# Performance work log

Hardware: AMD Instinct MI355X
Metric: run time of the kernel (lower is better)

## Reference

```python
import jax, jax.numpy as jnp
import numpy as np
import math

# Config: 8 packed images, each a 32x32 patch grid (t=1) -> equal seglen 1024
NSEG, GH, GW = 8, 32, 32
L = GH * GW            # 1024 tokens per segment
S = NSEG * L           # 8192 packed tokens
H, NH = 1024, 16
HD = H // NH           # 64, head dim (rope dim), divisible by 4
MLP = 4096
THETA = 10000.0


def _make_rope_cos_sin():
    # Rope2DPosEmb._precompute_freqs_cis for a (GH, GW) grid, dim=HD
    flat = np.arange(L, dtype=np.float32)
    x_pos = flat % GW
    y_pos = flat // GW
    dim_range = np.arange(0, HD, 4, dtype=np.float32)[: HD // 4]
    freqs = 1.0 / THETA ** (dim_range / HD)          # [HD//4]
    x_f = np.outer(x_pos, freqs)                     # [L, HD//4]
    y_f = np.outer(y_pos, freqs)
    # interleave x/y angles per frequency -> [L, HD//2]
    ang = np.stack([x_f, y_f], axis=-1).reshape(L, HD // 2)
    ang = np.tile(ang, (NSEG, 1))                    # same grid repeated per image
    return jnp.asarray(np.cos(ang)), jnp.asarray(np.sin(ang))


def setup_inputs() -> dict:
    key = jax.random.key(0)
    ks = jax.random.split(key, 8)
    cos, sin = _make_rope_cos_sin()
    inp = {
        "x": jax.random.normal(ks[0], (S, H), jnp.float32),
        "wqkv": jax.random.normal(ks[1], (3 * H, H), jnp.float32) * math.sqrt(1.0 / H),
        "wo": jax.random.normal(ks[2], (H, H), jnp.float32) * math.sqrt(1.0 / H),
        "ln0_g": jnp.ones((H,), jnp.float32),
        "ln0_b": jnp.zeros((H,), jnp.float32),
        "ln1_g": jnp.ones((H,), jnp.float32),
        "ln1_b": jnp.zeros((H,), jnp.float32),
        "fc0_w": jax.random.normal(ks[3], (MLP, H), jnp.float32) * math.sqrt(2.0 / H),
        "fc0_b": jnp.zeros((MLP,), jnp.float32),
        "fc1_w": jax.random.normal(ks[4], (H, MLP), jnp.float32) * math.sqrt(2.0 / MLP),
        "fc1_b": jnp.zeros((H,), jnp.float32),
        "rope_cos": cos,
        "rope_sin": sin,
        "cu_seqlens": jnp.arange(NSEG + 1, dtype=jnp.int32) * L,
    }
    return inp


def _layernorm(x, g, b, eps=1e-5):
    m = x.mean(-1, keepdims=True)
    v = ((x - m) ** 2).mean(-1, keepdims=True)
    return (x - m) * jax.lax.rsqrt(v + eps) * g + b


def _apply_rope(x, cos, sin):
    # x: [S, NH, HD]; cos/sin: [S, HD//2]. Complex mult on (even, odd) pairs.
    xr = x.reshape(S, NH, HD // 2, 2)
    x0, x1 = xr[..., 0], xr[..., 1]
    c = cos[:, None, :]
    s = sin[:, None, :]
    o0 = x0 * c - x1 * s
    o1 = x0 * s + x1 * c
    return jnp.stack([o0, o1], axis=-1).reshape(S, NH, HD)


def reference(x, wqkv, wo, ln0_g, ln0_b, ln1_g, ln1_b,
              fc0_w, fc0_b, fc1_w, fc1_b, rope_cos, rope_sin, cu_seqlens):
    # --- attention branch (pre-norm) ---
    h = _layernorm(x, ln0_g, ln0_b)
    qkv = (h @ wqkv.T).reshape(S, 3, NH, HD)
    q, k, v = qkv[:, 0], qkv[:, 1], qkv[:, 2]
    q = _apply_rope(q, rope_cos, rope_sin)
    k = _apply_rope(k, rope_cos, rope_sin)
    # block-diagonal varlen attention: equal-length segments -> reshape
    qb = q.reshape(NSEG, L, NH, HD)
    kb = k.reshape(NSEG, L, NH, HD)
    vb = v.reshape(NSEG, L, NH, HD)
    scores = jnp.einsum("blhd,bmhd->bhlm", qb, kb) / math.sqrt(HD)
    p = jax.nn.softmax(scores.astype(jnp.float32), axis=-1).astype(x.dtype)
    attn = jnp.einsum("bhlm,bmhd->blhd", p, vb).reshape(S, H)
    x = x + attn @ wo.T
    # --- MLP branch (pre-norm) ---
    h2 = _layernorm(x, ln1_g, ln1_b)
    mlp = jax.nn.gelu(h2 @ fc0_w.T + fc0_b, approximate=False) @ fc1_w.T + fc1_b
    return x + mlp
```

## Files before the change

kernel.cpp:

```cpp
#include <hip/hip_runtime.h>
#include <math.h>


typedef __bf16 bf16x8 __attribute__((ext_vector_type(8)));
typedef float f32x4 __attribute__((ext_vector_type(4)));
typedef float f32x16 __attribute__((ext_vector_type(16)));
typedef unsigned int u32;

__device__ __forceinline__ unsigned short f2b(float f) {
  unsigned u = __float_as_uint(f);
  return (unsigned short)((u + 0x7FFFu + ((u >> 16) & 1u)) >> 16);
}
__device__ __forceinline__ float b2f(unsigned short h) {
  return __uint_as_float(((unsigned)h) << 16);
}
__device__ __forceinline__ void async_ld16(const void* g, void* l) {
  __builtin_amdgcn_global_load_lds((__attribute__((address_space(1))) void*)g,
                                   (__attribute__((address_space(3))) void*)l,
                                   16, 0, 0);
}
__device__ __forceinline__ float exp2fast(float x) {
#if __has_builtin(__builtin_amdgcn_exp2f)
  return __builtin_amdgcn_exp2f(x);
#else
  return exp2f(x);
#endif
}
__device__ __forceinline__ float rcpfast(float x) {
#if __has_builtin(__builtin_amdgcn_rcpf)
  return __builtin_amdgcn_rcpf(x);
#else
  return 1.0f / x;
#endif
}

__global__ __launch_bounds__(256) void castln_kernel(
    const float* __restrict__ w0, const float* __restrict__ w1,
    const float* __restrict__ w2, const float* __restrict__ w3,
    unsigned short* __restrict__ wdst,
    const float* __restrict__ x, const float* __restrict__ g,
    const float* __restrict__ bt, unsigned short* __restrict__ hout) {
  __shared__ float red[8];
  const int blk = blockIdx.x;
  if (blk < 12288) {
    const int t = blk * 256 + threadIdx.x;
    const float* src;
    int off;
    if (t < 786432) { src = w0; off = t; }
    else if (t < 1048576) { src = w1; off = t - 786432; }
    else if (t < 2097152) { src = w2; off = t - 1048576; }
    else { src = w3; off = t - 2097152; }
    const float4 v = ((const float4*)src)[off];
    ushort4 o;
    o.x = f2b(v.x); o.y = f2b(v.y); o.z = f2b(v.z); o.w = f2b(v.w);
    ((ushort4*)wdst)[t] = o;
    return;
  }
  const int row = blk - 12288, t = threadIdx.x;
  const float4 v = ((const float4*)(x + (size_t)row * 1024))[t];
  float s = v.x + v.y + v.z + v.w;
  float s2 = v.x * v.x + v.y * v.y + v.z * v.z + v.w * v.w;
#pragma unroll
  for (int m = 1; m < 64; m <<= 1) {
    s += __shfl_xor(s, m, 64);
    s2 += __shfl_xor(s2, m, 64);
  }
  if ((t & 63) == 0) { red[t >> 6] = s; red[4 + (t >> 6)] = s2; }
  __syncthreads();
  const float ts = red[0] + red[1] + red[2] + red[3];
  const float ts2 = red[4] + red[5] + red[6] + red[7];
  const float mean = ts * (1.f / 1024.f);
  const float var = ts2 * (1.f / 1024.f) - mean * mean;
  const float inv = rsqrtf(var + 1e-5f);
  const float4 gv = ((const float4*)g)[t];
  const float4 bv = ((const float4*)bt)[t];
  ushort4 o;
  o.x = f2b((v.x - mean) * inv * gv.x + bv.x);
  o.y = f2b((v.y - mean) * inv * gv.y + bv.y);
  o.z = f2b((v.z - mean) * inv * gv.z + bv.z);
  o.w = f2b((v.w - mean) * inv * gv.w + bv.w);
  ((ushort4*)hout)[(size_t)row * 256 + t] = o;
}

__global__ __launch_bounds__(256) void ln_kernel(const float* __restrict__ x,
                                                 const float* __restrict__ g,
                                                 const float* __restrict__ bt,
                                                 unsigned short* __restrict__ out) {
  __shared__ float red[8];
  const int row = blockIdx.x, t = threadIdx.x;
  const float4 v = ((const float4*)(x + (size_t)row * 1024))[t];
  float s = v.x + v.y + v.z + v.w;
  float s2 = v.x * v.x + v.y * v.y + v.z * v.z + v.w * v.w;
#pragma unroll
  for (int m = 1; m < 64; m <<= 1) {
    s += __shfl_xor(s, m, 64);
    s2 += __shfl_xor(s2, m, 64);
  }
  if ((t & 63) == 0) { red[t >> 6] = s; red[4 + (t >> 6)] = s2; }
  __syncthreads();
  const float ts = red[0] + red[1] + red[2] + red[3];
  const float ts2 = red[4] + red[5] + red[6] + red[7];
  const float mean = ts * (1.f / 1024.f);
  const float var = ts2 * (1.f / 1024.f) - mean * mean;
  const float inv = rsqrtf(var + 1e-5f);
  const float4 gv = ((const float4*)g)[t];
  const float4 bv = ((const float4*)bt)[t];
  ushort4 o;
  o.x = f2b((v.x - mean) * inv * gv.x + bv.x);
  o.y = f2b((v.y - mean) * inv * gv.y + bv.y);
  o.z = f2b((v.z - mean) * inv * gv.z + bv.z);
  o.w = f2b((v.w - mean) * inv * gv.w + bv.w);
  ((ushort4*)out)[(size_t)row * 256 + t] = o;
}

template <int MODE, int NBN>
__global__ __launch_bounds__(256) void gemm_bt(
    const unsigned short* __restrict__ A, const unsigned short* __restrict__ B,
    int M, int N, int K, float* __restrict__ outf, unsigned short* __restrict__ outb,
    const float* __restrict__ res, const float* __restrict__ bias) {
  __shared__ __align__(16) unsigned short As[128 * 32];
  __shared__ __align__(16) unsigned short Bs[128 * 32];
  const int bid = blockIdx.x;
  const int j8 = bid & 7, g = bid >> 3;
  const int bm = ((g / NBN) * 8 + j8) * 128;
  const int bn = (g % NBN) * 128;
  const int t = threadIdx.x, wave = t >> 6, lane = t & 63;
  const int quad = lane >> 4, l16 = lane & 15;
  const int wm = (wave >> 1) * 64, wn = (wave & 1) * 64;
  const int srow = lane >> 2;
  const int scol = (((lane & 3) ^ ((lane >> 3) & 3)) * 8);
  const unsigned short* Ag0 = A + (size_t)(bm + wave * 32 + srow) * K + scol;
  const unsigned short* Ag1 = Ag0 + (size_t)16 * K;
  const unsigned short* Bg0 = B + (size_t)(bn + wave * 32 + srow) * K + scol;
  const unsigned short* Bg1 = Bg0 + (size_t)16 * K;
  unsigned short* Al = As + wave * 1024;
  unsigned short* Bl = Bs + wave * 1024;
  const int swg = (l16 >> 1) & 3;
  f32x4 acc[4][4] = {};
  for (int k0 = 0; k0 < K; k0 += 32) {
    async_ld16(Ag0 + k0, Al);
    async_ld16(Ag1 + k0, Al + 512);
    async_ld16(Bg0 + k0, Bl);
    async_ld16(Bg1 + k0, Bl + 512);
    __syncthreads();
    bf16x8 af[4], bfv[4];
#pragma unroll
    for (int i = 0; i < 4; i++)
      af[i] = *(const bf16x8*)(As + (wm + i * 16 + l16) * 32 + (quad ^ swg) * 8);
#pragma unroll
    for (int jj = 0; jj < 4; jj++)
      bfv[jj] = *(const bf16x8*)(Bs + (wn + jj * 16 + l16) * 32 + (quad ^ swg) * 8);
#pragma unroll
    for (int i = 0; i < 4; i++)
#pragma unroll
      for (int jj = 0; jj < 4; jj++)
        acc[i][jj] = __builtin_amdgcn_mfma_f32_16x16x32_bf16(af[i], bfv[jj], acc[i][jj], 0, 0, 0);
    __syncthreads();
  }
#pragma unroll
  for (int i = 0; i < 4; i++)
#pragma unroll
    for (int jj = 0; jj < 4; jj++)
#pragma unroll
      for (int r = 0; r < 4; r++) {
        const int m = bm + wm + i * 16 + quad * 4 + r;
        const int n = bn + wn + jj * 16 + l16;
        const size_t idx = (size_t)m * N + n;
        const float v = acc[i][jj][r];
        if (MODE == 1) {
          outf[idx] = v + res[idx];
        } else if (MODE == 2) {
          const float z = v + bias[n];
          const float u = z * (0.7978845608f + 0.03567740814f * z * z);
          const float e = fminf(u * 2.885390082f, 80.f);
          const float tt = exp2fast(e);
          outb[idx] = f2b(z * tt * rcpfast(tt + 1.0f));
        } else if (MODE == 3) {
          outf[idx] = v + bias[n] + res[idx];
        } else {
          outb[idx] = f2b(v);
        }
      }
}

__device__ __forceinline__ u32 rope2(u32 in, float c, float sn, float sc) {
  const float a = b2f((unsigned short)(in & 0xffff));
  const float b = b2f((unsigned short)(in >> 16));
  return (u32)f2b((a * c - b * sn) * sc) | ((u32)f2b((a * sn + b * c) * sc) << 16);
}
__global__ __launch_bounds__(256) void ropevt_kernel(const unsigned short* __restrict__ qkv,
                                                     const float* __restrict__ cb,
                                                     const float* __restrict__ sb,
                                                     unsigned short* __restrict__ qh,
                                                     unsigned short* __restrict__ kh,
                                                     unsigned short* __restrict__ vt) {
  __shared__ unsigned short tile[64][72];
  const int blk = blockIdx.x;
  if (blk < 4096) {
    const int tid = blk * 256 + threadIdx.x;
    const int ii = tid & 7, head = (tid >> 3) & 15, s = tid >> 7;
    const float4 cv = *(const float4*)(cb + s * 32 + ii * 4);
    const float4 sv = *(const float4*)(sb + s * 32 + ii * 4);
    const unsigned short* base = qkv + (size_t)s * 3072 + head * 64 + ii * 8;
    const uint4 qa = *(const uint4*)base;
    const uint4 ka = *(const uint4*)(base + 1024);
    const int seg = s >> 10, l = s & 1023;
    const size_t o = ((size_t)((seg * 16 + head) * 1024 + l)) * 64 + ii * 8;
    const float QSC = 0.125f * 1.44269504f;
    uint4 qo, ko;
    qo.x = rope2(qa.x, cv.x, sv.x, QSC); ko.x = rope2(ka.x, cv.x, sv.x, 1.f);
    qo.y = rope2(qa.y, cv.y, sv.y, QSC); ko.y = rope2(ka.y, cv.y, sv.y, 1.f);
    qo.z = rope2(qa.z, cv.z, sv.z, QSC); ko.z = rope2(ka.z, cv.z, sv.z, 1.f);
    qo.w = rope2(qa.w, cv.w, sv.w, QSC); ko.w = rope2(ka.w, cv.w, sv.w, 1.f);
    *(uint4*)(qh + o) = qo;
    *(uint4*)(kh + o) = ko;
    return;
  }
  const int b = blk - 4096;
  const int lt = b & 15, head = (b >> 4) & 15, seg = b >> 8;
  const int t = threadIdx.x;
  const int r = t >> 2, c0 = (t & 3) * 16;
  const unsigned short* src =
      qkv + ((size_t)(seg * 1024 + lt * 64 + r)) * 3072 + 2048 + head * 64 + c0;
#pragma unroll
  for (int k = 0; k < 16; k++) tile[r][c0 + k] = src[k];
  __syncthreads();
  unsigned short* dst =
      vt + ((size_t)((seg * 16 + head) * 64 + r)) * 1024 + lt * 64 + c0;
#pragma unroll
  for (int k = 0; k < 16; k++) dst[k] = tile[c0 + k][r];
}

__global__ __launch_bounds__(256) void attn_kernel(const unsigned short* __restrict__ qh,
                                                   const unsigned short* __restrict__ kh,
                                                   const unsigned short* __restrict__ vt,
                                                   unsigned short* __restrict__ out) {
  __shared__ __align__(16) unsigned short Qs[128 * 64];
  __shared__ __align__(16) unsigned short Ks[64 * 64];
  __shared__ __align__(16) unsigned short Vs[64 * 64];
  __shared__ float wl[128];
  const int b = blockIdx.x;
  const int head = b & 15, seg = (b >> 4) & 7, qt = b >> 7;
  const int t = threadIdx.x, wave = t >> 6, lane = t & 63;
  const int h = lane >> 5, q31 = lane & 31;
  const size_t sh = (size_t)(seg * 16 + head);
  const unsigned short* qbase = qh + (sh * 1024 + (size_t)qt * 128) * 64;
  const unsigned short* kbase = kh + sh * 1024 * 64;
  const unsigned short* vbase = vt + sh * 64 * 1024;
  const int r8 = lane >> 3;
  const int c8 = ((lane & 7) ^ (r8 & 7)) * 8;
#pragma unroll
  for (int cc = 0; cc < 4; cc++) {
    const int chunk = wave * 4 + cc;
    async_ld16(qbase + (size_t)(chunk * 8 + r8) * 64 + c8, Qs + chunk * 512);
  }
  const int qrow_l = wave * 32 + q31;
  const int qsw = qrow_l & 7;
  bf16x8 qf[4];
  float lsum = 0.f;
  f32x16 oacc[2] = {};

  for (int kt = 0; kt < 16; kt++) {
    const int ch0 = wave * 2;
    async_ld16(kbase + (size_t)(kt * 64 + ch0 * 8 + r8) * 64 + c8, Ks + ch0 * 512);
    async_ld16(kbase + (size_t)(kt * 64 + ch0 * 8 + 8 + r8) * 64 + c8, Ks + ch0 * 512 + 512);
    async_ld16(vbase + (size_t)(ch0 * 8 + r8) * 1024 + kt * 64 + c8, Vs + ch0 * 512);
    async_ld16(vbase + (size_t)(ch0 * 8 + 8 + r8) * 1024 + kt * 64 + c8, Vs + ch0 * 512 + 512);
    __syncthreads();
    if (kt == 0) {
#pragma unroll
      for (int ks = 0; ks < 4; ks++)
        qf[ks] = *(const bf16x8*)(Qs + qrow_l * 64 + (((2 * ks + h) ^ qsw)) * 8);
    }
    f32x16 st[2] = {{}, {}};
#pragma unroll
    for (int T = 0; T < 2; T++) {
      const int krow = 32 * T + q31;
      const int ksw = krow & 7;
#pragma unroll
      for (int ks = 0; ks < 4; ks++) {
        const bf16x8 kf = *(const bf16x8*)(Ks + krow * 64 + (((2 * ks + h) ^ ksw)) * 8);
        st[T] = __builtin_amdgcn_mfma_f32_32x32x16_bf16(kf, qf[ks], st[T], 0, 0, 0);
      }
    }
    u32 pk[2][4][2];
#pragma unroll
    for (int T = 0; T < 2; T++)
#pragma unroll
      for (int g = 0; g < 4; g++)
#pragma unroll
        for (int e = 0; e < 2; e++) {
          const float plo = exp2fast(st[T][4 * g + 2 * e]);
          const float phi = exp2fast(st[T][4 * g + 2 * e + 1]);
          lsum += plo + phi;
          pk[T][g][e] = (u32)f2b(plo) | ((u32)f2b(phi) << 16);
        }
    u32 rcv[2][4];
#pragma unroll
    for (int T = 0; T < 2; T++) {
      const u32 p0 = h ? pk[T][0][0] : pk[T][1][0];
      const u32 p1 = h ? pk[T][0][1] : pk[T][1][1];
      const u32 p2 = h ? pk[T][2][0] : pk[T][3][0];
      const u32 p3 = h ? pk[T][2][1] : pk[T][3][1];
      rcv[T][0] = (u32)__shfl_xor((int)p0, 32, 64);
      rcv[T][1] = (u32)__shfl_xor((int)p1, 32, 64);
      rcv[T][2] = (u32)__shfl_xor((int)p2, 32, 64);
      rcv[T][3] = (u32)__shfl_xor((int)p3, 32, 64);
    }
#pragma unroll
    for (int tt = 0; tt < 4; tt++) {
      const int T = tt >> 1, uu = tt & 1;
      union { u32 u[4]; bf16x8 v; } af;
      if (h == 0) {
        af.u[0] = pk[T][2 * uu][0];
        af.u[1] = pk[T][2 * uu][1];
        af.u[2] = rcv[T][2 * uu];
        af.u[3] = rcv[T][2 * uu + 1];
      } else {
        af.u[0] = rcv[T][2 * uu];
        af.u[1] = rcv[T][2 * uu + 1];
        af.u[2] = pk[T][2 * uu + 1][0];
        af.u[3] = pk[T][2 * uu + 1][1];
      }
#pragma unroll
      for (int ot = 0; ot < 2; ot++) {
        const int vrow = 32 * ot + q31;
        const int vsw = vrow & 7;
        const bf16x8 bv = *(const bf16x8*)(Vs + vrow * 64 + (((2 * tt + h) ^ vsw)) * 8);
        oacc[ot] = __builtin_amdgcn_mfma_f32_32x32x16_bf16(af.v, bv, oacc[ot], 0, 0, 0);
      }
    }
    __syncthreads();
  }
  lsum += __shfl_xor(lsum, 32, 64);
  if (h == 0) wl[wave * 32 + q31] = lsum;
  const int qglob = seg * 1024 + qt * 128 + wave * 32;
#pragma unroll
  for (int g = 0; g < 4; g++) {
    const float4 lv = *(const float4*)&wl[wave * 32 + 8 * g + 4 * h];
#pragma unroll
    for (int m = 0; m < 4; m++) {
      const int r16 = 4 * g + m;
      const int qrow = qglob + m + 8 * g + 4 * h;
      const float invl = rcpfast((&lv.x)[m]);
#pragma unroll
      for (int ot = 0; ot < 2; ot++)
        out[(size_t)qrow * 1024 + head * 64 + 32 * ot + q31] = f2b(oacc[ot][r16] * invl);
    }
  }
}

extern "C" void kernel_launch(void* const* d_in, const int* in_sizes, int n_in,
                              void* d_out, int out_size, void* d_ws, size_t ws_size,
                              hipStream_t stream) {
  (void)in_sizes; (void)n_in; (void)out_size; (void)ws_size;
  const float* x    = (const float*)d_in[0];
  const float* wqkv = (const float*)d_in[1];
  const float* wo   = (const float*)d_in[2];
  const float* ln0g = (const float*)d_in[3];
  const float* ln0b = (const float*)d_in[4];
  const float* ln1g = (const float*)d_in[5];
  const float* ln1b = (const float*)d_in[6];
  const float* fc0w = (const float*)d_in[7];
  const float* fc0b = (const float*)d_in[8];
  const float* fc1w = (const float*)d_in[9];
  const float* fc1b = (const float*)d_in[10];
  const float* rc   = (const float*)d_in[11];
  const float* rsn  = (const float*)d_in[12];
  float* out = (float*)d_out;
  char* w = (char*)d_ws;
  const size_t MB = 1u << 20;
  unsigned short* hb    = (unsigned short*)(w + 0);
  unsigned short* bqkv  = (unsigned short*)(w + 16 * MB);
  unsigned short* bwo   = (unsigned short*)(w + 22 * MB);
  unsigned short* bfc0  = (unsigned short*)(w + 24 * MB);
  unsigned short* bfc1  = (unsigned short*)(w + 32 * MB);
  unsigned short* qhb   = (unsigned short*)(w + 40 * MB);
  unsigned short* khb   = (unsigned short*)(w + 56 * MB);
  unsigned short* vtb   = (unsigned short*)(w + 72 * MB);
  unsigned short* attnb = (unsigned short*)(w + 88 * MB);
  unsigned short* qkvb  = (unsigned short*)(w + 104 * MB);
  unsigned short* midb  = (unsigned short*)(w + 104 * MB);

  castln_kernel<<<20480, 256, 0, stream>>>(wqkv, wo, fc0w, fc1w, bqkv,
                                           x, ln0g, ln0b, hb);
  gemm_bt<4, 24><<<1536, 256, 0, stream>>>(hb, bqkv, 8192, 3072, 1024,
                                           nullptr, qkvb, nullptr, nullptr);
  ropevt_kernel<<<6144, 256, 0, stream>>>(qkvb, rc, rsn, qhb, khb, vtb);
  attn_kernel<<<1024, 256, 0, stream>>>(qhb, khb, vtb, attnb);
  gemm_bt<1, 8><<<512, 256, 0, stream>>>(attnb, bwo, 8192, 1024, 1024,
                                         out, nullptr, x, nullptr);
  ln_kernel<<<8192, 256, 0, stream>>>(out, ln1g, ln1b, hb);
  gemm_bt<2, 32><<<2048, 256, 0, stream>>>(hb, bfc0, 8192, 4096, 1024,
                                           nullptr, midb, nullptr, fc0b);
  gemm_bt<3, 8><<<512, 256, 0, stream>>>(midb, bfc1, 8192, 1024, 4096,
                                         out, nullptr, out, fc1b);
}
```

Before: 526.5 us.

## Rewrite GEMMs with 256-row tiles, 8 waves, double-buffered LDS prefetch

Replaces the 128x128, 4-wave, single-buffered GEMM with a 256xBN tile (BN=128 or 256) run by 512 threads, a K-step of 64, and two LDS buffers. Global-to-LDS async loads for the next stage are issued while MFMAs run on the current one, using explicit vmcnt waits, barriers and setprio to manage overlap. The goal is to hide memory latency and raise operand reuse per LDS load. In exchange it uses much more LDS (up to 128KB per block), which may limit occupancy, and it launches fewer blocks, which can leave CUs idle on the smaller GEMMs.

```diff
diff --git a/kernel.cpp b/kernel.cpp
--- a/kernel.cpp
+++ b/kernel.cpp
@@ -113,60 +113,114 @@
   ((ushort4*)out)[(size_t)row * 256 + t] = o;
 }
 
-template <int MODE, int NBN>
-__global__ __launch_bounds__(256) void gemm_bt(
+template <int MODE, int NBN, int BN>
+__global__ __launch_bounds__(512, 2) void gemm_bt8(
     const unsigned short* __restrict__ A, const unsigned short* __restrict__ B,
     int M, int N, int K, float* __restrict__ outf, unsigned short* __restrict__ outb,
     const float* __restrict__ res, const float* __restrict__ bias) {
-  __shared__ __align__(16) unsigned short As[128 * 32];
-  __shared__ __align__(16) unsigned short Bs[128 * 32];
+  constexpr int NBI = BN / 64;
+  constexpr int WN_WAVES = BN / 64;
+  constexpr int WM_WAVES = 8 / WN_WAVES;
+  constexpr int M_REP = (256 / WM_WAVES) / 16;
+  constexpr int N_REP = 4;
+  __shared__ __align__(16) unsigned short As[2][256 * 64];
+  __shared__ __align__(16) unsigned short Bs[2][BN * 64];
   const int bid = blockIdx.x;
   const int j8 = bid & 7, g = bid >> 3;
-  const int bm = ((g / NBN) * 8 + j8) * 128;
-  const int bn = (g % NBN) * 128;
+  const int bm = ((g / NBN) * 8 + j8) * 256;
+  const int bn = (g % NBN) * BN;
   const int t = threadIdx.x, wave = t >> 6, lane = t & 63;
   const int quad = lane >> 4, l16 = lane & 15;
-  const int wm = (wave >> 1) * 64, wn = (wave & 1) * 64;
-  const int srow = lane >> 2;
-  const int scol = (((lane & 3) ^ ((lane >> 3) & 3)) * 8);
-  const unsigned short* Ag0 = A + (size_t)(bm + wave * 32 + srow) * K + scol;
-  const unsigned short* Ag1 = Ag0 + (size_t)16 * K;
-  const unsigned short* Bg0 = B + (size_t)(bn + wave * 32 + srow) * K + scol;
-  const unsigned short* Bg1 = Bg0 + (size_t)16 * K;
-  unsigned short* Al = As + wave * 1024;
-  unsigned short* Bl = Bs + wave * 1024;
-  const int swg = (l16 >> 1) & 3;
-  f32x4 acc[4][4] = {};
-  for (int k0 = 0; k0 < K; k0 += 32) {
-    async_ld16(Ag0 + k0, Al);
-    async_ld16(Ag1 + k0, Al + 512);
-    async_ld16(Bg0 + k0, Bl);
-    async_ld16(Bg1 + k0, Bl + 512);
-    __syncthreads();
-    bf16x8 af[4], bfv[4];
-#pragma unroll
-    for (int i = 0; i < 4; i++)
-      af[i] = *(const bf16x8*)(As + (wm + i * 16 + l16) * 32 + (quad ^ swg) * 8);
-#pragma unroll
-    for (int jj = 0; jj < 4; jj++)
-      bfv[jj] = *(const bf16x8*)(Bs + (wn + jj * 16 + l16) * 32 + (quad ^ swg) * 8);
-#pragma unroll
-    for (int i = 0; i < 4; i++)
-#pragma unroll
-      for (int jj = 0; jj < 4; jj++)
-        acc[i][jj] = __builtin_amdgcn_mfma_f32_16x16x32_bf16(af[i], bfv[jj], acc[i][jj], 0, 0, 0);
-    __syncthreads();
-  }
-#pragma unroll
-  for (int i = 0; i < 4; i++)
-#pragma unroll
-    for (int jj = 0; jj < 4; jj++)
+  const int wm = (wave / WN_WAVES) * (M_REP * 16);
+  const int wn = (wave % WN_WAVES) * 64;
+  const int l8 = lane >> 3;
+  const int cs = ((lane & 7) ^ (l8 & 7)) * 8;
+  const unsigned short* Ag[4];
+  unsigned short* Al[4];
+#pragma unroll
+  for (int i = 0; i < 4; i++) {
+    const int r = wave * 32 + i * 8;
+    Ag[i] = A + (size_t)(bm + r + l8) * K + cs;
+    Al[i] = &As[0][r * 64];
+  }
+  const unsigned short* Bg[NBI];
+  unsigned short* Bl[NBI];
+#pragma unroll
+  for (int i = 0; i < NBI; i++) {
+    const int r = wave * (NBI * 8) + i * 8;
+    Bg[i] = B + (size_t)(bn + r + l8) * K + cs;
+    Bl[i] = &Bs[0][r * 64];
+  }
+#define STAGE(bi, k0)                                                        \
+  do {                                                                       \
+    _Pragma("unroll") for (int i_ = 0; i_ < 4; i_++)                         \
+        async_ld16(Ag[i_] + (k0), Al[i_] + (bi) * (256 * 64));               \
+    _Pragma("unroll") for (int i_ = 0; i_ < NBI; i_++)                       \
+        async_ld16(Bg[i_] + (k0), Bl[i_] + (bi) * (BN * 64));                \
+  } while (0)
+
+  f32x4 acc[M_REP][N_REP] = {};
+  const int NT = K >> 6;
+  const int swk = l16 & 7;
+  STAGE(0, 0);
+  STAGE(1, 64);
+  if (BN == 256) asm volatile("s_waitcnt vmcnt(8)" ::: "memory");
+  else           asm volatile("s_waitcnt vmcnt(6)" ::: "memory");
+  __builtin_amdgcn_sched_barrier(0);
+  __builtin_amdgcn_s_barrier();
+  __builtin_amdgcn_sched_barrier(0);
+  int k0 = 128;
+  for (int tI = 0; tI < NT; ++tI) {
+    const int cur = tI & 1;
+    const unsigned short* Ab = &As[cur][0];
+    const unsigned short* Bb = &Bs[cur][0];
+#pragma unroll
+    for (int ks = 0; ks < 2; ks++) {
+      bf16x8 af[M_REP], bfv[N_REP];
+#pragma unroll
+      for (int i = 0; i < M_REP; i++)
+        af[i] = *(const bf16x8*)(Ab + (wm + i * 16 + l16) * 64 +
+                                 (((ks * 4 + quad) ^ swk) * 8));
+#pragma unroll
+      for (int j = 0; j < N_REP; j++)
+        bfv[j] = *(const bf16x8*)(Bb + (wn + j * 16 + l16) * 64 +
+                                  (((ks * 4 + quad) ^ swk) * 8));
+      __builtin_amdgcn_s_setprio(1);
+#pragma unroll
+      for (int j = 0; j < N_REP; j++)
+#pragma unroll
+        for (int i = 0; i < M_REP; i++)
+          acc[i][j] = __builtin_amdgcn_mfma_f32_16x16x32_bf16(af[i], bfv[j],
+                                                              acc[i][j], 0, 0, 0);
+      __builtin_amdgcn_s_setprio(0);
+    }
+    if (tI + 1 == NT) break;
+    __builtin_amdgcn_sched_barrier(0);
+    __builtin_amdgcn_s_barrier();
+    __builtin_amdgcn_sched_barrier(0);
+    if (tI + 2 < NT) {
+      STAGE(cur, k0);
+      k0 += 64;
+      if (BN == 256) asm volatile("s_waitcnt vmcnt(8)" ::: "memory");
+      else           asm volatile("s_waitcnt vmcnt(6)" ::: "memory");
+    } else {
+      asm volatile("s_waitcnt vmcnt(0)" ::: "memory");
+    }
+    __builtin_amdgcn_sched_barrier(0);
+    __builtin_amdgcn_s_barrier();
+    __builtin_amdgcn_sched_barrier(0);
+  }
+#undef STAGE
+#pragma unroll
+  for (int i = 0; i < M_REP; i++)
+#pragma unroll
+    for (int j = 0; j < N_REP; j++)
 #pragma unroll
       for (int r = 0; r < 4; r++) {
         const int m = bm + wm + i * 16 + quad * 4 + r;
-        const int n = bn + wn + jj * 16 + l16;
+        const int n = bn + wn + j * 16 + l16;
         const size_t idx = (size_t)m * N + n;
-        const float v = acc[i][jj][r];
+        const float v = acc[i][j][r];
         if (MODE == 1) {
           outf[idx] = v + res[idx];
         } else if (MODE == 2) {
@@ -384,15 +438,15 @@
 
   castln_kernel<<<20480, 256, 0, stream>>>(wqkv, wo, fc0w, fc1w, bqkv,
                                            x, ln0g, ln0b, hb);
-  gemm_bt<4, 24><<<1536, 256, 0, stream>>>(hb, bqkv, 8192, 3072, 1024,
-                                           nullptr, qkvb, nullptr, nullptr);
+  gemm_bt8<4, 24, 128><<<768, 512, 0, stream>>>(hb, bqkv, 8192, 3072, 1024,
+                                                nullptr, qkvb, nullptr, nullptr);
   ropevt_kernel<<<6144, 256, 0, stream>>>(qkvb, rc, rsn, qhb, khb, vtb);
   attn_kernel<<<1024, 256, 0, stream>>>(qhb, khb, vtb, attnb);
-  gemm_bt<1, 8><<<512, 256, 0, stream>>>(attnb, bwo, 8192, 1024, 1024,
-                                         out, nullptr, x, nullptr);
+  gemm_bt8<1, 8, 128><<<256, 512, 0, stream>>>(attnb, bwo, 8192, 1024, 1024,
+                                               out, nullptr, x, nullptr);
   ln_kernel<<<8192, 256, 0, stream>>>(out, ln1g, ln1b, hb);
-  gemm_bt<2, 32><<<2048, 256, 0, stream>>>(hb, bfc0, 8192, 4096, 1024,
-                                           nullptr, midb, nullptr, fc0b);
-  gemm_bt<3, 8><<<512, 256, 0, stream>>>(midb, bfc1, 8192, 1024, 4096,
-                                         out, nullptr, out, fc1b);
-}
+  gemm_bt8<2, 16, 256><<<512, 512, 0, stream>>>(hb, bfc0, 8192, 4096, 1024,
+                                                nullptr, midb, nullptr, fc0b);
+  gemm_bt8<3, 8, 128><<<256, 512, 0, stream>>>(midb, bfc1, 8192, 1024, 4096,
+                                               out, nullptr, out, fc1b);
+}
```

Result: faster. 508.7 us (-3.4%).

## Replace GEMM with larger-tile, 8-wave, double-buffered async-load pipelined kernel

Applied to the files above, without the earlier changes.

Replaces the 128x128, 4-wave GEMM with a templated kernel using 256-wide N tiles and 128 or 256 M tiles, 8 waves per block, and a K step of 64 split into two 32-wide stages. The stages are double-buffered in LDS. Global-to-LDS async loads for later K steps are issued while MFMAs run, with explicit vmcnt waits, barriers and setprio around the MFMA bursts. This is meant to hide global load latency and raise data reuse per block. In exchange it uses much more LDS per block, uses fewer blocks (which can underfill the CUs for the N=1024 GEMMs), and depends on hand-counted waitcnts being correct.

```diff
diff --git a/kernel.cpp b/kernel.cpp
--- a/kernel.cpp
+++ b/kernel.cpp
@@ -113,52 +113,117 @@
   ((ushort4*)out)[(size_t)row * 256 + t] = o;
 }
 
-template <int MODE, int NBN>
-__global__ __launch_bounds__(256) void gemm_bt(
+template <int MODE, int NBN, int BM>
+__global__ __launch_bounds__(512, 2) void gemm_p8(
     const unsigned short* __restrict__ A, const unsigned short* __restrict__ B,
     int M, int N, int K, float* __restrict__ outf, unsigned short* __restrict__ outb,
     const float* __restrict__ res, const float* __restrict__ bias) {
-  __shared__ __align__(16) unsigned short As[128 * 32];
-  __shared__ __align__(16) unsigned short Bs[128 * 32];
+  constexpr int NPH = (BM == 256) ? 4 : 2;
+  constexpr int NF = (BM == 256) ? 2 : 4;
+  constexpr int M_REP = BM / 32;
+  constexpr int AI = BM / 128;
+  constexpr int VST = AI + 2;
+  constexpr int STG2 = (BM == 256) ? 2 : 1;
+  __shared__ __align__(16) unsigned short As[2][2][BM * 32];
+  __shared__ __align__(16) unsigned short Bs[2][2][256 * 32];
   const int bid = blockIdx.x;
   const int j8 = bid & 7, g = bid >> 3;
-  const int bm = ((g / NBN) * 8 + j8) * 128;
-  const int bn = (g % NBN) * 128;
+  const int bm = ((g / NBN) * 8 + j8) * BM;
+  const int bn = (g % NBN) * 256;
   const int t = threadIdx.x, wave = t >> 6, lane = t & 63;
   const int quad = lane >> 4, l16 = lane & 15;
-  const int wm = (wave >> 1) * 64, wn = (wave & 1) * 64;
-  const int srow = lane >> 2;
-  const int scol = (((lane & 3) ^ ((lane >> 3) & 3)) * 8);
-  const unsigned short* Ag0 = A + (size_t)(bm + wave * 32 + srow) * K + scol;
-  const unsigned short* Ag1 = Ag0 + (size_t)16 * K;
-  const unsigned short* Bg0 = B + (size_t)(bn + wave * 32 + srow) * K + scol;
-  const unsigned short* Bg1 = Bg0 + (size_t)16 * K;
-  unsigned short* Al = As + wave * 1024;
-  unsigned short* Bl = Bs + wave * 1024;
-  const int swg = (l16 >> 1) & 3;
-  f32x4 acc[4][4] = {};
-  for (int k0 = 0; k0 < K; k0 += 32) {
-    async_ld16(Ag0 + k0, Al);
-    async_ld16(Ag1 + k0, Al + 512);
-    async_ld16(Bg0 + k0, Bl);
-    async_ld16(Bg1 + k0, Bl + 512);
-    __syncthreads();
-    bf16x8 af[4], bfv[4];
-#pragma unroll
-    for (int i = 0; i < 4; i++)
-      af[i] = *(const bf16x8*)(As + (wm + i * 16 + l16) * 32 + (quad ^ swg) * 8);
-#pragma unroll
-    for (int jj = 0; jj < 4; jj++)
-      bfv[jj] = *(const bf16x8*)(Bs + (wn + jj * 16 + l16) * 32 + (quad ^ swg) * 8);
-#pragma unroll
-    for (int i = 0; i < 4; i++)
-#pragma unroll
-      for (int jj = 0; jj < 4; jj++)
-        acc[i][jj] = __builtin_amdgcn_mfma_f32_16x16x32_bf16(af[i], bfv[jj], acc[i][jj], 0, 0, 0);
-    __syncthreads();
-  }
-#pragma unroll
-  for (int i = 0; i < 4; i++)
+  const int wm = (wave >> 2) * (M_REP * 16);
+  const int wn = (wave & 3) * 64;
+  const int r16 = lane >> 2;
+  const int cs8 = (((lane & 3) ^ ((lane >> 3) & 3)) * 8);
+  const unsigned short* AgS[AI];
+  unsigned short* AlS[AI];
+#pragma unroll
+  for (int i = 0; i < AI; i++) {
+    const int r0 = wave * (AI * 16) + i * 16;
+    AgS[i] = A + (size_t)(bm + r0 + r16) * K + cs8;
+    AlS[i] = &As[0][0][r0 * 32];
+  }
+  const unsigned short* BgS[2];
+  unsigned short* BlS[2];
+#pragma unroll
+  for (int i = 0; i < 2; i++) {
+    const int r0 = wave * 32 + i * 16;
+    BgS[i] = B + (size_t)(bn + r0 + r16) * K + cs8;
+    BlS[i] = &Bs[0][0][r0 * 32];
+  }
+#define STG(bi, kt, ks)                                                      \
+  do {                                                                       \
+    _Pragma("unroll") for (int i_ = 0; i_ < AI; i_++)                        \
+        async_ld16(AgS[i_] + (size_t)(kt) * 64 + (ks) * 32,                  \
+                   AlS[i_] + ((bi) * 2 + (ks)) * (BM * 32));                 \
+    _Pragma("unroll") for (int i_ = 0; i_ < 2; i_++)                         \
+        async_ld16(BgS[i_] + (size_t)(kt) * 64 + (ks) * 32,                  \
+                   BlS[i_] + ((bi) * 2 + (ks)) * (256 * 32));                \
+  } while (0)
+
+  f32x4 acc[M_REP][4] = {};
+  const int NT = K >> 6;
+  const int rq = ((quad ^ ((l16 >> 1) & 3)) * 8);
+  STG(0, 0, 0);
+  STG(0, 0, 1);
+  STG(1, 1, 0);
+  __builtin_amdgcn_sched_barrier(0);
+  if (BM == 256) asm volatile("s_waitcnt vmcnt(4)" ::: "memory");
+  else           asm volatile("s_waitcnt vmcnt(3)" ::: "memory");
+  __builtin_amdgcn_sched_barrier(0);
+  __builtin_amdgcn_s_barrier();
+  __builtin_amdgcn_sched_barrier(0);
+
+  bf16x8 af[M_REP];
+  for (int u = 0; u < NT; ++u) {
+    const int buf = u & 1, nbuf = buf ^ 1;
+#pragma unroll
+    for (int p = 0; p < NPH; ++p) {
+      const int ks = (NPH == 4) ? (p >> 1) : p;
+      const int j0 = (NPH == 4) ? (p & 1) * 2 : 0;
+      const unsigned short* Ab = &As[buf][ks][0];
+      const unsigned short* Bb = &Bs[buf][ks][0];
+      if (NPH == 2 || (p & 1) == 0) {
+#pragma unroll
+        for (int i = 0; i < M_REP; i++)
+          af[i] = *(const bf16x8*)(Ab + (wm + i * 16 + l16) * 32 + rq);
+      }
+      bf16x8 bfv[NF];
+#pragma unroll
+      for (int jj = 0; jj < NF; jj++)
+        bfv[jj] = *(const bf16x8*)(Bb + (wn + (j0 + jj) * 16 + l16) * 32 + rq);
+      if (p == 0 && u + 1 < NT) STG(nbuf, u + 1, 1);
+      if (p == STG2 && u + 2 < NT) STG(buf, u + 2, 0);
+      __builtin_amdgcn_sched_barrier(0);
+      __builtin_amdgcn_s_barrier();
+      asm volatile("s_waitcnt lgkmcnt(0)" ::: "memory");
+      __builtin_amdgcn_sched_barrier(0);
+      __builtin_amdgcn_s_setprio(1);
+#pragma unroll
+      for (int jj = 0; jj < NF; jj++)
+#pragma unroll
+        for (int i = 0; i < M_REP; i++)
+          acc[i][j0 + jj] = __builtin_amdgcn_mfma_f32_16x16x32_bf16(
+              af[i], bfv[jj], acc[i][j0 + jj], 0, 0, 0);
+      __builtin_amdgcn_s_setprio(0);
+      if (p == NPH - 1 && u + 1 < NT) {
+        __builtin_amdgcn_sched_barrier(0);
+        if (u + 2 < NT) {
+          if (BM == 256) asm volatile("s_waitcnt vmcnt(4)" ::: "memory");
+          else           asm volatile("s_waitcnt vmcnt(3)" ::: "memory");
+        } else {
+          asm volatile("s_waitcnt vmcnt(0)" ::: "memory");
+        }
+      }
+      __builtin_amdgcn_sched_barrier(0);
+      __builtin_amdgcn_s_barrier();
+      __builtin_amdgcn_sched_barrier(0);
+    }
+  }
+#undef STG
+#pragma unroll
+  for (int i = 0; i < M_REP; i++)
 #pragma unroll
     for (int jj = 0; jj < 4; jj++)
 #pragma unroll
@@ -384,15 +449,15 @@
 
   castln_kernel<<<20480, 256, 0, stream>>>(wqkv, wo, fc0w, fc1w, bqkv,
                                            x, ln0g, ln0b, hb);
-  gemm_bt<4, 24><<<1536, 256, 0, stream>>>(hb, bqkv, 8192, 3072, 1024,
-                                           nullptr, qkvb, nullptr, nullptr);
+  gemm_p8<4, 12, 256><<<384, 512, 0, stream>>>(hb, bqkv, 8192, 3072, 1024,
+                                               nullptr, qkvb, nullptr, nullptr);
   ropevt_kernel<<<6144, 256, 0, stream>>>(qkvb, rc, rsn, qhb, khb, vtb);
   attn_kernel<<<1024, 256, 0, stream>>>(qhb, khb, vtb, attnb);
-  gemm_bt<1, 8><<<512, 256, 0, stream>>>(attnb, bwo, 8192, 1024, 1024,
-                                         out, nullptr, x, nullptr);
+  gemm_p8<1, 4, 128><<<256, 512, 0, stream>>>(attnb, bwo, 8192, 1024, 1024,
+                                              out, nullptr, x, nullptr);
   ln_kernel<<<8192, 256, 0, stream>>>(out, ln1g, ln1b, hb);
-  gemm_bt<2, 32><<<2048, 256, 0, stream>>>(hb, bfc0, 8192, 4096, 1024,
-                                           nullptr, midb, nullptr, fc0b);
-  gemm_bt<3, 8><<<512, 256, 0, stream>>>(midb, bfc1, 8192, 1024, 4096,
-                                         out, nullptr, out, fc1b);
-}
+  gemm_p8<2, 16, 256><<<512, 512, 0, stream>>>(hb, bfc0, 8192, 4096, 1024,
+                                               nullptr, midb, nullptr, fc0b);
+  gemm_p8<3, 4, 128><<<256, 512, 0, stream>>>(midb, bfc1, 8192, 1024, 4096,
+                                              out, nullptr, out, fc1b);
+}
```

After: 492.9 us. 6.4% less time.

## Triple-buffer GEMM K-loop with async prefetch and add 256-row tiles

Applied to the files above, without the earlier changes.

Replaces the single-buffered GEMM, which used two block barriers per K step, with a three-stage LDS ring. Global-to-LDS loads run two tiles ahead, with explicit vmcnt waits, one barrier per step, and raised wave priority around the MFMA block. The QKV and FC0 GEMMs now use 256-row tiles with 512 threads, which halves the grid and reuses each B tile across more rows. LDS use per block triples, which may limit occupancy and relies on hand-placed waitcnt and barrier sequencing being correct.

```diff
diff --git a/kernel.cpp b/kernel.cpp
--- a/kernel.cpp
+++ b/kernel.cpp
@@ -113,50 +113,100 @@
   ((ushort4*)out)[(size_t)row * 256 + t] = o;
 }
 
-template <int MODE, int NBN>
-__global__ __launch_bounds__(256) void gemm_bt(
+template <int MODE, int NBN, int BM>
+__global__ __launch_bounds__(BM == 256 ? 512 : 256, BM == 256 ? 4 : 3)
+void gemm_tb(
     const unsigned short* __restrict__ A, const unsigned short* __restrict__ B,
     int M, int N, int K, float* __restrict__ outf, unsigned short* __restrict__ outb,
     const float* __restrict__ res, const float* __restrict__ bias) {
-  __shared__ __align__(16) unsigned short As[128 * 32];
-  __shared__ __align__(16) unsigned short Bs[128 * 32];
+  constexpr int WAVES = (BM == 256) ? 8 : 4;
+  constexpr int BI = 8 / WAVES;
+  constexpr int ASZ = BM * 32;
+  constexpr int BSZ = 128 * 32;
+  __shared__ __align__(16) unsigned short As[3 * ASZ];
+  __shared__ __align__(16) unsigned short Bs[3 * BSZ];
   const int bid = blockIdx.x;
   const int j8 = bid & 7, g = bid >> 3;
-  const int bm = ((g / NBN) * 8 + j8) * 128;
+  const int bm = ((g / NBN) * 8 + j8) * BM;
   const int bn = (g % NBN) * 128;
   const int t = threadIdx.x, wave = t >> 6, lane = t & 63;
   const int quad = lane >> 4, l16 = lane & 15;
   const int wm = (wave >> 1) * 64, wn = (wave & 1) * 64;
-  const int srow = lane >> 2;
-  const int scol = (((lane & 3) ^ ((lane >> 3) & 3)) * 8);
-  const unsigned short* Ag0 = A + (size_t)(bm + wave * 32 + srow) * K + scol;
-  const unsigned short* Ag1 = Ag0 + (size_t)16 * K;
-  const unsigned short* Bg0 = B + (size_t)(bn + wave * 32 + srow) * K + scol;
-  const unsigned short* Bg1 = Bg0 + (size_t)16 * K;
-  unsigned short* Al = As + wave * 1024;
-  unsigned short* Bl = Bs + wave * 1024;
+  const int r16 = lane >> 2;
+  const int cs8 = (((lane & 3) ^ ((lane >> 3) & 3)) * 8);
+  const unsigned short* Ag[2];
+  unsigned short* Al[2];
+#pragma unroll
+  for (int i = 0; i < 2; i++) {
+    const int ch = wave * 2 + i;
+    Ag[i] = A + (size_t)(bm + ch * 16 + r16) * K + cs8;
+    Al[i] = As + ch * (16 * 32);
+  }
+  const unsigned short* Bg[BI];
+  unsigned short* Bl[BI];
+#pragma unroll
+  for (int i = 0; i < BI; i++) {
+    const int ch = wave * BI + i;
+    Bg[i] = B + (size_t)(bn + ch * 16 + r16) * K + cs8;
+    Bl[i] = Bs + ch * (16 * 32);
+  }
+#define STG(tt, bi)                                                          \
+  do {                                                                       \
+    const size_t ko_ = (size_t)(tt) * 32;                                    \
+    _Pragma("unroll") for (int i_ = 0; i_ < 2; i_++)                         \
+        async_ld16(Ag[i_] + ko_, Al[i_] + (bi) * ASZ);                       \
+    _Pragma("unroll") for (int i_ = 0; i_ < BI; i_++)                        \
+        async_ld16(Bg[i_] + ko_, Bl[i_] + (bi) * BSZ);                       \
+  } while (0)
+
+  f32x4 acc[4][4] = {};
+  const int NT = K >> 5;
   const int swg = (l16 >> 1) & 3;
-  f32x4 acc[4][4] = {};
-  for (int k0 = 0; k0 < K; k0 += 32) {
-    async_ld16(Ag0 + k0, Al);
-    async_ld16(Ag1 + k0, Al + 512);
-    async_ld16(Bg0 + k0, Bl);
-    async_ld16(Bg1 + k0, Bl + 512);
-    __syncthreads();
+  STG(0, 0);
+  STG(1, 1);
+  if constexpr (BM == 256) asm volatile("s_waitcnt vmcnt(3)" ::: "memory");
+  else                     asm volatile("s_waitcnt vmcnt(4)" ::: "memory");
+  __builtin_amdgcn_sched_barrier(0);
+  __builtin_amdgcn_s_barrier();
+  __builtin_amdgcn_sched_barrier(0);
+  int cb = 0, sb = 2;
+  for (int tt = 0; tt < NT; ++tt) {
+    if (tt + 2 < NT) STG(tt + 2, sb);
+    const unsigned short* Ab = As + cb * ASZ;
+    const unsigned short* Bb = Bs + cb * BSZ;
     bf16x8 af[4], bfv[4];
 #pragma unroll
     for (int i = 0; i < 4; i++)
-      af[i] = *(const bf16x8*)(As + (wm + i * 16 + l16) * 32 + (quad ^ swg) * 8);
-#pragma unroll
-    for (int jj = 0; jj < 4; jj++)
-      bfv[jj] = *(const bf16x8*)(Bs + (wn + jj * 16 + l16) * 32 + (quad ^ swg) * 8);
-#pragma unroll
-    for (int i = 0; i < 4; i++)
-#pragma unroll
-      for (int jj = 0; jj < 4; jj++)
-        acc[i][jj] = __builtin_amdgcn_mfma_f32_16x16x32_bf16(af[i], bfv[jj], acc[i][jj], 0, 0, 0);
-    __syncthreads();
-  }
+      af[i] = *(const bf16x8*)(Ab + (wm + i * 16 + l16) * 32 + (quad ^ swg) * 8);
+#pragma unroll
+    for (int j = 0; j < 4; j++)
+      bfv[j] = *(const bf16x8*)(Bb + (wn + j * 16 + l16) * 32 + (quad ^ swg) * 8);
+    asm volatile("s_waitcnt lgkmcnt(0)" ::: "memory");
+    __builtin_amdgcn_sched_barrier(0);
+    __builtin_amdgcn_s_setprio(1);
+#pragma unroll
+    for (int j = 0; j < 4; j++)
+#pragma unroll
+      for (int i = 0; i < 4; i++)
+        acc[i][j] = __builtin_amdgcn_mfma_f32_16x16x32_bf16(af[i], bfv[j],
+                                                            acc[i][j], 0, 0, 0);
+    __builtin_amdgcn_s_setprio(0);
+    if (tt + 1 < NT) {
+      __builtin_amdgcn_sched_barrier(0);
+      if (tt + 2 < NT) {
+        if constexpr (BM == 256) asm volatile("s_waitcnt vmcnt(3)" ::: "memory");
+        else                     asm volatile("s_waitcnt vmcnt(4)" ::: "memory");
+      } else {
+        asm volatile("s_waitcnt vmcnt(0)" ::: "memory");
+      }
+      __builtin_amdgcn_sched_barrier(0);
+      __builtin_amdgcn_s_barrier();
+      __builtin_amdgcn_sched_barrier(0);
+    }
+    cb = (cb == 2) ? 0 : cb + 1;
+    sb = (sb == 2) ? 0 : sb + 1;
+  }
+#undef STG
 #pragma unroll
   for (int i = 0; i < 4; i++)
 #pragma unroll
@@ -173,8 +223,8 @@
           const float z = v + bias[n];
           const float u = z * (0.7978845608f + 0.03567740814f * z * z);
           const float e = fminf(u * 2.885390082f, 80.f);
-          const float tt = exp2fast(e);
-          outb[idx] = f2b(z * tt * rcpfast(tt + 1.0f));
+          const float tt2 = exp2fast(e);
+          outb[idx] = f2b(z * tt2 * rcpfast(tt2 + 1.0f));
         } else if (MODE == 3) {
           outf[idx] = v + bias[n] + res[idx];
         } else {
@@ -384,15 +434,15 @@
 
   castln_kernel<<<20480, 256, 0, stream>>>(wqkv, wo, fc0w, fc1w, bqkv,
                                            x, ln0g, ln0b, hb);
-  gemm_bt<4, 24><<<1536, 256, 0, stream>>>(hb, bqkv, 8192, 3072, 1024,
-                                           nullptr, qkvb, nullptr, nullptr);
+  gemm_tb<4, 24, 256><<<768, 512, 0, stream>>>(hb, bqkv, 8192, 3072, 1024,
+                                               nullptr, qkvb, nullptr, nullptr);
   ropevt_kernel<<<6144, 256, 0, stream>>>(qkvb, rc, rsn, qhb, khb, vtb);
   attn_kernel<<<1024, 256, 0, stream>>>(qhb, khb, vtb, attnb);
-  gemm_bt<1, 8><<<512, 256, 0, stream>>>(attnb, bwo, 8192, 1024, 1024,
-                                         out, nullptr, x, nullptr);
+  gemm_tb<1, 8, 128><<<512, 256, 0, stream>>>(attnb, bwo, 8192, 1024, 1024,
+                                              out, nullptr, x, nullptr);
   ln_kernel<<<8192, 256, 0, stream>>>(out, ln1g, ln1b, hb);
-  gemm_bt<2, 32><<<2048, 256, 0, stream>>>(hb, bfc0, 8192, 4096, 1024,
-                                           nullptr, midb, nullptr, fc0b);
-  gemm_bt<3, 8><<<512, 256, 0, stream>>>(midb, bfc1, 8192, 1024, 4096,
-                                         out, nullptr, out, fc1b);
-}
+  gemm_tb<2, 32, 256><<<1024, 512, 0, stream>>>(hb, bfc0, 8192, 4096, 1024,
+                                                nullptr, midb, nullptr, fc0b);
+  gemm_tb<3, 8, 128><<<512, 256, 0, stream>>>(midb, bfc1, 8192, 1024, 4096,
+                                              out, nullptr, out, fc1b);
+}
```

New measurement: 500.6 us. -4.9%, faster.
